# Kernel optimization log

Hardware: AMD Instinct MI355X
Metric: run time of the kernel (lower is better)

The kernel has to match this reference:

```python
import jax, jax.numpy as jnp
import numpy as np

T = 20.0  # temperature
SCALE = 0.3

def reference(outputs1, outputs2, outputs3, outputs4, outputs5, outputs6, outputs7, outputs8, targets):
    # preds: [M=8, B, C] tempered softmaxes
    logits = jnp.stack([outputs1, outputs2, outputs3, outputs4,
                        outputs5, outputs6, outputs7, outputs8], axis=0)
    preds = jax.nn.softmax(logits / T, axis=-1)
    # center over class dim (Pearson correlation per sample per model)
    v = preds - jnp.mean(preds, axis=-1, keepdims=True)
    v = v / jnp.sqrt(jnp.sum(v * v, axis=-1, keepdims=True))  # unit-norm rows
    # Gram over model pairs: [B, M, M]
    G = jnp.einsum('mbc,nbc->bmn', v, v)
    M = G.shape[-1]
    # sum over upper triangle (j<k); diagonal entries are exactly 1 pre-normalization
    d = (jnp.sum(G, axis=(1, 2)) - jnp.trace(G, axis1=1, axis2=2)) * 0.5  # [B]
    loss = SCALE * d
    return jnp.mean(loss)

def setup_inputs() -> dict:
    key = jax.random.key(0)
    ks = jax.random.split(key, 9)
    B, C = 4096, 1000
    inp = {f'outputs{i+1}': jax.random.normal(ks[i], (B, C), dtype=jnp.float32)
           for i in range(8)}
    inp['targets'] = jax.random.randint(ks[8], (B,), 0, C, dtype=jnp.int64)
    return inp
```

## Files before the change

### kernel.cpp

```cpp
#include <hip/hip_runtime.h>
#include <math.h>


constexpr int NC   = 1000;
constexpr int NC4  = 250;
constexpr int NM   = 8;
constexpr float TINV = 1.0f / 20.0f;
constexpr float INVC = 1.0f / (float)NC;

__device__ __forceinline__ float waveSum(float v) {
#pragma unroll
    for (int o = 32; o > 0; o >>= 1) v += __shfl_xor(v, o, 64);
    return v;
}
__device__ __forceinline__ double waveSumD(double v) {
#pragma unroll
    for (int o = 32; o > 0; o >>= 1) v += __shfl_xor(v, o, 64);
    return v;
}

__global__ __launch_bounds__(256, 4) void div8_main(
    const float* __restrict__ in0, const float* __restrict__ in1,
    const float* __restrict__ in2, const float* __restrict__ in3,
    const float* __restrict__ in4, const float* __restrict__ in5,
    const float* __restrict__ in6, const float* __restrict__ in7,
    float* __restrict__ part, int B)
{
    const int wid  = threadIdx.x >> 6;
    const int lane = threadIdx.x & 63;
    const int b    = blockIdx.x * 4 + wid;
    if (b >= B) return;
    const bool act3 = lane < (NC4 - 3 * 64);

    const float* rows[NM] = {
        in0 + (size_t)b * NC, in1 + (size_t)b * NC,
        in2 + (size_t)b * NC, in3 + (size_t)b * NC,
        in4 + (size_t)b * NC, in5 + (size_t)b * NC,
        in6 + (size_t)b * NC, in7 + (size_t)b * NC };

    float4 t4[4], s4[4];
#pragma unroll
    for (int j = 0; j < 4; ++j) {
        t4[j] = make_float4(0.f, 0.f, 0.f, 0.f);
        s4[j] = make_float4(0.f, 0.f, 0.f, 0.f);
    }

#pragma unroll
    for (int m = 0; m < NM; ++m) {
        const float4* p = reinterpret_cast<const float4*>(rows[m]);

        float4 e[4];
#pragma unroll
        for (int j = 0; j < 4; ++j) {
            float4 v = (j < 3) ? p[lane + 64 * j]
                     : (act3 ? p[lane + 192]
                             : make_float4(-INFINITY, -INFINITY, -INFINITY, -INFINITY));
            e[j].x = __expf(v.x * TINV);
            e[j].y = __expf(v.y * TINV);
            e[j].z = __expf(v.z * TINV);
            e[j].w = __expf(v.w * TINV);
        }

        float s = 0.f;
#pragma unroll
        for (int j = 0; j < 4; ++j)
            s += (e[j].x + e[j].y) + (e[j].z + e[j].w);
        const float S  = waveSum(s);
        const float SC = S * INVC;

        float qq = 0.f;
#pragma unroll
        for (int j = 0; j < 4; ++j) {
            if (j == 3 && !act3) continue;
            float u0 = e[j].x - SC;
            float u1 = e[j].y - SC;
            float u2 = e[j].z - SC;
            float u3 = e[j].w - SC;
            qq = fmaf(u0, u0, fmaf(u1, u1, fmaf(u2, u2, fmaf(u3, u3, qq))));
        }
        const float qt = waveSum(qq);
        const float rm = 1.0f / sqrtf(qt);
        const float bmv = -SC * rm;

#pragma unroll
        for (int j = 0; j < 4; ++j) {
            if (j == 3 && !act3) continue;
            float w;
            w = fmaf(e[j].x, rm, bmv); t4[j].x += w; s4[j].x = fmaf(w, w, s4[j].x);
            w = fmaf(e[j].y, rm, bmv); t4[j].y += w; s4[j].y = fmaf(w, w, s4[j].y);
            w = fmaf(e[j].z, rm, bmv); t4[j].z += w; s4[j].z = fmaf(w, w, s4[j].z);
            w = fmaf(e[j].w, rm, bmv); t4[j].w += w; s4[j].w = fmaf(w, w, s4[j].w);
        }
    }

    double cr = 0.0;
#pragma unroll
    for (int j = 0; j < 4; ++j) {
        cr += (double)fmaf(t4[j].x, t4[j].x, -s4[j].x);
        cr += (double)fmaf(t4[j].y, t4[j].y, -s4[j].y);
        cr += (double)fmaf(t4[j].z, t4[j].z, -s4[j].z);
        cr += (double)fmaf(t4[j].w, t4[j].w, -s4[j].w);
    }
    cr = waveSumD(cr);
    if (lane == 0) part[b] = (float)cr;
}

__global__ __launch_bounds__(256) void div8_final(
    const float* __restrict__ part, float* __restrict__ out, int B)
{
    const int t = threadIdx.x;
    double acc = 0.0;
    for (int i = t; i < B; i += 256) acc += (double)part[i];
    acc = waveSumD(acc);
    __shared__ double redd[4];
    if ((t & 63) == 0) redd[t >> 6] = acc;
    __syncthreads();
    if (t == 0) {
        double tot = (redd[0] + redd[1]) + (redd[2] + redd[3]);
        out[0] = (float)(tot * (0.5 * 0.3 / (double)B));
    }
}

extern "C" void kernel_launch(void* const* d_in, const int* in_sizes, int n_in,
                              void* d_out, int out_size, void* d_ws, size_t ws_size,
                              hipStream_t stream)
{
    const float* a0 = (const float*)d_in[0];
    const float* a1 = (const float*)d_in[1];
    const float* a2 = (const float*)d_in[2];
    const float* a3 = (const float*)d_in[3];
    const float* a4 = (const float*)d_in[4];
    const float* a5 = (const float*)d_in[5];
    const float* a6 = (const float*)d_in[6];
    const float* a7 = (const float*)d_in[7];
    const int B = in_sizes[0] / NC;

    float* part = (float*)d_ws;

    const int grid = (B + 3) / 4;
    div8_main<<<grid, 256, 0, stream>>>(a0, a1, a2, a3, a4, a5, a6, a7, part, B);
    div8_final<<<1, 256, 0, stream>>>(part, (float*)d_out, B);
}
```

Before: 36.73 us.

## Compute per-sample Gram via raw moment accumulation in a single pass

Replaces the per-model normalize-then-accumulate pass with a single pass that accumulates raw sums and all 36 pairwise cross-products of exp(x/T)-1. Centering and normalization then happen algebraically on lane 0 in double precision. This removes the two dependent wave reductions per model and interleaves loads across all eight models. In exchange it does 36 FMAs per element plus 44 wave reductions, which raises register pressure. The shift by -1 is meant to limit cancellation, but float accumulation of raw moments is still less accurate than the centered form.

```diff
diff --git a/kernel.cpp b/kernel.cpp
--- a/kernel.cpp
+++ b/kernel.cpp
@@ -5,8 +5,8 @@
 constexpr int NC   = 1000;
 constexpr int NC4  = 250;
 constexpr int NM   = 8;
-constexpr float TINV = 1.0f / 20.0f;
-constexpr float INVC = 1.0f / (float)NC;
+constexpr int NPAIR = NM * (NM + 1) / 2;
+__device__ constexpr float KEXP = 0.072134752044448169f;
 
 __device__ __forceinline__ float waveSum(float v) {
 #pragma unroll
@@ -17,6 +17,9 @@
 #pragma unroll
     for (int o = 32; o > 0; o >>= 1) v += __shfl_xor(v, o, 64);
     return v;
+}
+__device__ __forceinline__ constexpr int tidx(int m, int n) {
+    return m * (2 * NM - m + 1) / 2 + (n - m);
 }
 
 __global__ __launch_bounds__(256, 4) void div8_main(
@@ -38,71 +41,76 @@
         in4 + (size_t)b * NC, in5 + (size_t)b * NC,
         in6 + (size_t)b * NC, in7 + (size_t)b * NC };
 
-    float4 t4[4], s4[4];
+    float D[NPAIR];
+    float t[NM];
+#pragma unroll
+    for (int k = 0; k < NPAIR; ++k) D[k] = 0.f;
+#pragma unroll
+    for (int m = 0; m < NM; ++m) t[m] = 0.f;
+
 #pragma unroll
     for (int j = 0; j < 4; ++j) {
-        t4[j] = make_float4(0.f, 0.f, 0.f, 0.f);
-        s4[j] = make_float4(0.f, 0.f, 0.f, 0.f);
+        float4 u[NM];
+#pragma unroll
+        for (int m = 0; m < NM; ++m) {
+            const float4* p = reinterpret_cast<const float4*>(rows[m]);
+            if (j < 3) {
+                float4 v = p[lane + 64 * j];
+                u[m].x = exp2f(v.x * KEXP) - 1.f;
+                u[m].y = exp2f(v.y * KEXP) - 1.f;
+                u[m].z = exp2f(v.z * KEXP) - 1.f;
+                u[m].w = exp2f(v.w * KEXP) - 1.f;
+            } else if (act3) {
+                float4 v = p[lane + 192];
+                u[m].x = exp2f(v.x * KEXP) - 1.f;
+                u[m].y = exp2f(v.y * KEXP) - 1.f;
+                u[m].z = exp2f(v.z * KEXP) - 1.f;
+                u[m].w = exp2f(v.w * KEXP) - 1.f;
+            } else {
+                u[m] = make_float4(0.f, 0.f, 0.f, 0.f);
+            }
+        }
+#pragma unroll
+        for (int comp = 0; comp < 4; ++comp) {
+            float us[NM];
+#pragma unroll
+            for (int m = 0; m < NM; ++m)
+                us[m] = (comp == 0) ? u[m].x : (comp == 1) ? u[m].y
+                      : (comp == 2) ? u[m].z : u[m].w;
+#pragma unroll
+            for (int m = 0; m < NM; ++m) {
+                t[m] += us[m];
+#pragma unroll
+                for (int n = m; n < NM; ++n)
+                    D[tidx(m, n)] = fmaf(us[m], us[n], D[tidx(m, n)]);
+            }
+        }
     }
 
 #pragma unroll
-    for (int m = 0; m < NM; ++m) {
-        const float4* p = reinterpret_cast<const float4*>(rows[m]);
+    for (int k = 0; k < NPAIR; ++k) D[k] = waveSum(D[k]);
+#pragma unroll
+    for (int m = 0; m < NM; ++m) t[m] = waveSum(t[m]);
 
-        float4 e[4];
+    if (lane == 0) {
+        constexpr double INVC_D = 1.0 / (double)NC;
+        double rm[NM];
 #pragma unroll
-        for (int j = 0; j < 4; ++j) {
-            float4 v = (j < 3) ? p[lane + 64 * j]
-                     : (act3 ? p[lane + 192]
-                             : make_float4(-INFINITY, -INFINITY, -INFINITY, -INFINITY));
-            e[j].x = __expf(v.x * TINV);
-            e[j].y = __expf(v.y * TINV);
-            e[j].z = __expf(v.z * TINV);
-            e[j].w = __expf(v.w * TINV);
+        for (int m = 0; m < NM; ++m) {
+            double q = (double)D[tidx(m, m)] - (double)t[m] * (double)t[m] * INVC_D;
+            rm[m] = 1.0 / sqrt(q);
         }
-
-        float s = 0.f;
+        double cr = 0.0;
 #pragma unroll
-        for (int j = 0; j < 4; ++j)
-            s += (e[j].x + e[j].y) + (e[j].z + e[j].w);
-        const float S  = waveSum(s);
-        const float SC = S * INVC;
-
-        float qq = 0.f;
+        for (int m = 0; m < NM; ++m)
 #pragma unroll
-        for (int j = 0; j < 4; ++j) {
-            if (j == 3 && !act3) continue;
-            float u0 = e[j].x - SC;
-            float u1 = e[j].y - SC;
-            float u2 = e[j].z - SC;
-            float u3 = e[j].w - SC;
-            qq = fmaf(u0, u0, fmaf(u1, u1, fmaf(u2, u2, fmaf(u3, u3, qq))));
-        }
-        const float qt = waveSum(qq);
-        const float rm = 1.0f / sqrtf(qt);
-        const float bmv = -SC * rm;
-
-#pragma unroll
-        for (int j = 0; j < 4; ++j) {
-            if (j == 3 && !act3) continue;
-            float w;
-            w = fmaf(e[j].x, rm, bmv); t4[j].x += w; s4[j].x = fmaf(w, w, s4[j].x);
-            w = fmaf(e[j].y, rm, bmv); t4[j].y += w; s4[j].y = fmaf(w, w, s4[j].y);
-            w = fmaf(e[j].z, rm, bmv); t4[j].z += w; s4[j].z = fmaf(w, w, s4[j].z);
-            w = fmaf(e[j].w, rm, bmv); t4[j].w += w; s4[j].w = fmaf(w, w, s4[j].w);
-        }
+            for (int n = m + 1; n < NM; ++n) {
+                double cov = (double)D[tidx(m, n)]
+                           - (double)t[m] * (double)t[n] * INVC_D;
+                cr += cov * rm[m] * rm[n];
+            }
+        part[b] = (float)(2.0 * cr);
     }
-
-    double cr = 0.0;
-#pragma unroll
-    for (int j = 0; j < 4; ++j) {
-        cr += (double)fmaf(t4[j].x, t4[j].x, -s4[j].x);
-        cr += (double)fmaf(t4[j].y, t4[j].y, -s4[j].y);
-        cr += (double)fmaf(t4[j].z, t4[j].z, -s4[j].z);
-        cr += (double)fmaf(t4[j].w, t4[j].w, -s4[j].w);
-    }
-    cr = waveSumD(cr);
-    if (lane == 0) part[b] = (float)cr;
 }
 
 __global__ __launch_bounds__(256) void div8_final(
```

Result: slower. 56.01 us (+52.5%).
